# Kernel tuning notes

Hardware: AMD Instinct MI355X
Metric: run time of the kernel (lower is better)

## Reference

```python
import jax, jax.numpy as jnp
import numpy as np

WIN = 7       # window_size (square)
SHIFT = 3     # shift_size
HEADS = 4
WS = WIN * WIN  # 49 tokens per window


def _rel_index():
    # Swin relative position index, shape (WS*WS,), static ints
    coords = np.stack(np.meshgrid(np.arange(WIN), np.arange(WIN), indexing='ij'))
    cf = coords.reshape(2, -1)
    rel = (cf[:, :, None] - cf[:, None, :]).transpose(1, 2, 0)  # (WS, WS, 2)
    rel[:, :, 0] += WIN - 1
    rel[:, :, 1] += WIN - 1
    rel[:, :, 0] *= 2 * WIN - 1
    return rel.sum(-1).reshape(-1)

_REL_IDX = jnp.asarray(_rel_index())


def _attn_mask(H, W):
    # shift mask per window, shape (num_windows, WS, WS), static
    m = np.zeros((H, W), np.float32)
    cnt = 0
    for h in ((0, -WIN), (-WIN, -SHIFT), (-SHIFT, None)):
        for w in ((0, -WIN), (-WIN, -SHIFT), (-SHIFT, None)):
            m[h[0]:h[1], w[0]:w[1]] = cnt
            cnt += 1
    m = m.reshape(H // WIN, WIN, W // WIN, WIN).transpose(0, 2, 1, 3).reshape(-1, WS)
    diff = m[:, None, :] - m[:, :, None]
    return np.where(diff == 0, 0.0, -100.0).astype(np.float32)


def setup_inputs() -> dict:
    key = jax.random.key(0)
    ks = jax.random.split(key, 6)
    C = 128
    return {
        'x': jax.random.normal(ks[0], (64, 56, 56, C), jnp.float32),
        'qkv_kernel': jax.random.normal(ks[1], (C, 3 * C), jnp.float32) * (C ** -0.5),
        'qkv_bias': jax.random.normal(ks[2], (3 * C,), jnp.float32) * 0.02,
        'proj_kernel': jax.random.normal(ks[3], (C, C), jnp.float32) * (C ** -0.5),
        'proj_bias': jax.random.normal(ks[4], (C,), jnp.float32) * 0.02,
        'rel_pos_table': jax.random.normal(ks[5], ((2 * WIN - 1) ** 2, HEADS), jnp.float32) * 0.02,
    }


def reference(x, qkv_kernel, qkv_bias, proj_kernel, proj_bias, rel_pos_table):
    B, H, W, C = x.shape
    nH, nW = H // WIN, W // WIN
    head_dim = C // HEADS

    # cyclic shift + window partition -> (B*nH*nW, WS, C)
    xs = jnp.roll(x, (-SHIFT, -SHIFT), axis=(1, 2))
    xw = xs.reshape(B, nH, WIN, nW, WIN, C).transpose(0, 1, 3, 2, 4, 5).reshape(B * nH * nW, WS, C)

    qkv = xw @ qkv_kernel + qkv_bias
    qkv = qkv.reshape(-1, WS, 3, HEADS, head_dim).transpose(2, 0, 3, 1, 4)  # (3, n, h, WS, d)
    q, k, v = qkv[0], qkv[1], qkv[2]

    attn = jnp.einsum('nhsd,nhtd->nhst', q * head_dim ** -0.5, k)

    # relative position bias: (1, heads, WS, WS)
    bias = rel_pos_table[_REL_IDX].reshape(WS, WS, HEADS).transpose(2, 0, 1)[None]
    attn = attn + bias

    # shift mask (static)
    mask = jnp.asarray(_attn_mask(H, W))  # (nH*nW, WS, WS)
    attn = attn.reshape(B, nH * nW, HEADS, WS, WS) + mask[None, :, None]
    attn = jax.nn.softmax(attn.reshape(-1, HEADS, WS, WS), axis=-1)

    out = jnp.einsum('nhst,nhtd->nhsd', attn, v).transpose(0, 2, 1, 3).reshape(-1, WS, C)
    out = out @ proj_kernel + proj_bias

    # window merge + reverse shift
    out = out.reshape(B, nH, nW, WIN, WIN, C).transpose(0, 1, 3, 2, 4, 5).reshape(B, H, W, C)
    return jnp.roll(out, (SHIFT, SHIFT), axis=(1, 2))
```

## Files before the change

### kernel.cpp

```cpp
#include <hip/hip_runtime.h>
#include <hip/hip_bf16.h>

#define WIN 7
#define SHIFT_SZ 3
#define WSQ 49
#define CH 128
#define HW 56
#define LOG2E 1.4426950408889634f
#define QSCALE (0.17677669529663687f * LOG2E)

typedef short s16x8 __attribute__((ext_vector_type(8)));
typedef short s16x4 __attribute__((ext_vector_type(4)));
typedef float f32x4 __attribute__((ext_vector_type(4)));


__global__ void prep_weights(const float* __restrict__ qkv_kernel,
                             const float* __restrict__ proj_kernel,
                             __hip_bfloat16* __restrict__ ws) {
  int idx = blockIdx.x * 256 + threadIdx.x;
  if (idx < 49152) {
    int n = idx >> 7, c = idx & 127;
    ws[idx] = __float2bfloat16(qkv_kernel[c * 384 + n]);
  }
  if (idx < 16384) {
    int n = idx >> 7, c = idx & 127;
    ws[49152 + idx] = __float2bfloat16(proj_kernel[c * 128 + n]);
  }
}

__global__ void prep_tbl(const float* __restrict__ rel_pos_table,
                         __hip_bfloat16* __restrict__ tbl) {
  int idx = blockIdx.x * 256 + threadIdx.x;
  int t = idx & 63;
  int s = (idx >> 6) & 63;
  int h = (idx >> 12) & 3;
  int cls = idx >> 14;
  float v;
  if (t >= WSQ) v = -43280.f;
  else if (s >= WSQ) v = 0.f;
  else {
    int i1 = s / 7, j1 = s % 7, i2 = t / 7, j2 = t % 7;
    int ridx = (i1 - i2 + 6) * 13 + (j1 - j2 + 6);
    float bias = rel_pos_table[ridx * 4 + h];
    int wyIs7 = cls >> 1, wxIs7 = cls & 1;
    int rh1 = wyIs7 ? (i1 < 4 ? 1 : 2) : 0;
    int rh2 = wyIs7 ? (i2 < 4 ? 1 : 2) : 0;
    int rw1 = wxIs7 ? (j1 < 4 ? 1 : 2) : 0;
    int rw2 = wxIs7 ? (j2 < 4 ? 1 : 2) : 0;
    float mask = (rh1 == rh2 && rw1 == rw2) ? 0.f : -100.f;
    v = (bias + mask) * LOG2E;
  }
  tbl[idx] = __float2bfloat16(v);
}


static __device__ __forceinline__ s16x8 ld2x64(const __hip_bfloat16* p) {
  s16x8 r;
  *(s16x4*)&r = *(const s16x4*)p;
  *(((s16x4*)&r) + 1) = *(const s16x4*)(p + 4);
  return r;
}

__launch_bounds__(512, 6)
__global__ void swin_attn(const float* __restrict__ x,
                          const float* __restrict__ qkv_bias,
                          const float* __restrict__ proj_bias,
                          const __hip_bfloat16* __restrict__ wqkvT,
                          const __hip_bfloat16* __restrict__ wprojT,
                          const __hip_bfloat16* __restrict__ tbl,
                          float* __restrict__ out) {
  __shared__ __align__(16) char smem[53248];
  __hip_bfloat16* a_lds  = (__hip_bfloat16*)smem;
  __hip_bfloat16* q_lds  = (__hip_bfloat16*)smem;
  __hip_bfloat16* k_lds  = (__hip_bfloat16*)(smem + 18432);
  __hip_bfloat16* vt_lds = (__hip_bfloat16*)(smem + 36864);
  __hip_bfloat16* p_lds  = (__hip_bfloat16*)smem;
  __hip_bfloat16* o_lds  = (__hip_bfloat16*)(smem + 36864);

  const int tid = threadIdx.x;
  const int lane = tid & 63;
  const int wv = tid >> 6;
  const int g = lane >> 4;
  const int c = lane & 15;
  const int e = c & 7;

  const int widx = blockIdx.x;
  const int b  = widx >> 6;
  const int wy = (widx >> 3) & 7;
  const int wx = widx & 7;
  const int mc = ((wy == 7) ? 2 : 0) + ((wx == 7) ? 1 : 0);

  for (int it = tid; it < 1024; it += 512) {
    int s = it >> 4;
    int l16 = it & 15;
    union { s16x8 v; __hip_bfloat16 h[8]; } u;
    if (s < WSQ) {
      int i = s / 7, j = s - i * 7;
      int hh = wy * 7 + i + SHIFT_SZ; if (hh >= HW) hh -= HW;
      int ww = wx * 7 + j + SHIFT_SZ; if (ww >= HW) ww -= HW;
      const float4* src = (const float4*)(x + (((b * HW + hh) * HW + ww) * CH + l16 * 8));
      float4 f0 = src[0], f1 = src[1];
      u.h[0] = __float2bfloat16(f0.x); u.h[1] = __float2bfloat16(f0.y);
      u.h[2] = __float2bfloat16(f0.z); u.h[3] = __float2bfloat16(f0.w);
      u.h[4] = __float2bfloat16(f1.x); u.h[5] = __float2bfloat16(f1.y);
      u.h[6] = __float2bfloat16(f1.z); u.h[7] = __float2bfloat16(f1.w);
    } else {
      #pragma unroll
      for (int q = 0; q < 8; ++q) u.h[q] = __float2bfloat16(0.f);
    }
    *(s16x8*)(a_lds + s * 128 + ((l16 ^ (s & 7)) * 8)) = u.v;
  }
  __syncthreads();

  {
    f32x4 acc_v[4];
    #pragma unroll
    for (int mt = 0; mt < 4; ++mt) acc_v[mt] = (f32x4){0.f, 0.f, 0.f, 0.f};
    #pragma unroll
    for (int kt = 0; kt < 4; ++kt) {
      s16x8 bv = *(const s16x8*)(wqkvT + (16 * (16 + wv) + c) * 128 + kt * 32 + g * 8);
      #pragma unroll
      for (int mt = 0; mt < 4; ++mt) {
        s16x8 af = *(const s16x8*)(a_lds + (16 * mt + c) * 128 + ((4 * kt + g) ^ e) * 8);
        acc_v[mt] = __builtin_amdgcn_mfma_f32_16x16x32_bf16(af, bv, acc_v[mt], 0, 0, 0);
      }
    }
    int hv = wv >> 1;
    int d = (wv & 1) * 16 + c;
    float bvb = qkv_bias[256 + wv * 16 + c];
    __hip_bfloat16* vdst = vt_lds + (hv * 32 + d) * 64;
    #pragma unroll
    for (int mt = 0; mt < 4; ++mt) {
      union { s16x4 v; __hip_bfloat16 h[4]; } u;
      #pragma unroll
      for (int r = 0; r < 4; ++r) u.h[r] = __float2bfloat16(acc_v[mt][r] + bvb);
      *(s16x4*)(vdst + ((2 * mt + (g >> 1)) ^ e) * 8 + (g & 1) * 4) = u.v;
    }
  }

  {
    f32x4 acc[2][4];
    #pragma unroll
    for (int ntl = 0; ntl < 2; ++ntl)
      #pragma unroll
      for (int mt = 0; mt < 4; ++mt) acc[ntl][mt] = (f32x4){0.f, 0.f, 0.f, 0.f};
    #pragma unroll
    for (int kt = 0; kt < 4; ++kt) {
      s16x8 af[4];
      #pragma unroll
      for (int mt = 0; mt < 4; ++mt)
        af[mt] = *(const s16x8*)(a_lds + (16 * mt + c) * 128 + ((4 * kt + g) ^ e) * 8);
      #pragma unroll
      for (int ntl = 0; ntl < 2; ++ntl) {
        s16x8 bf = *(const s16x8*)(wqkvT + (16 * (2 * wv + ntl) + c) * 128 + kt * 32 + g * 8);
        #pragma unroll
        for (int mt = 0; mt < 4; ++mt)
          acc[ntl][mt] = __builtin_amdgcn_mfma_f32_16x16x32_bf16(bf, af[mt], acc[ntl][mt], 0, 0, 0);
      }
    }
    const float scale = (wv < 4) ? QSCALE : 1.0f;
    if (wv >= 4) {
      #pragma unroll
      for (int ntl = 0; ntl < 2; ++ntl) {
        int qt = 2 * wv + ntl;
        int h = (qt >> 1) & 3;
        int d0 = (qt & 1) * 16 + 4 * g;
        float4 b4 = *(const float4*)(qkv_bias + qt * 16 + 4 * g);
        __hip_bfloat16* dst = k_lds + h * 2304 + d0;
        #pragma unroll
        for (int mt = 0; mt < 4; ++mt) {
          union { s16x4 v; __hip_bfloat16 h[4]; } u;
          u.h[0] = __float2bfloat16((acc[ntl][mt][0] + b4.x) * scale);
          u.h[1] = __float2bfloat16((acc[ntl][mt][1] + b4.y) * scale);
          u.h[2] = __float2bfloat16((acc[ntl][mt][2] + b4.z) * scale);
          u.h[3] = __float2bfloat16((acc[ntl][mt][3] + b4.w) * scale);
          *(s16x4*)(dst + (16 * mt + c) * 36) = u.v;
        }
      }
    }
    __syncthreads();
    if (wv < 4) {
      #pragma unroll
      for (int ntl = 0; ntl < 2; ++ntl) {
        int qt = 2 * wv + ntl;
        int h = (qt >> 1) & 3;
        int d0 = (qt & 1) * 16 + 4 * g;
        float4 b4 = *(const float4*)(qkv_bias + qt * 16 + 4 * g);
        __hip_bfloat16* dst = q_lds + h * 2304 + d0;
        #pragma unroll
        for (int mt = 0; mt < 4; ++mt) {
          union { s16x4 v; __hip_bfloat16 h[4]; } u;
          u.h[0] = __float2bfloat16((acc[ntl][mt][0] + b4.x) * scale);
          u.h[1] = __float2bfloat16((acc[ntl][mt][1] + b4.y) * scale);
          u.h[2] = __float2bfloat16((acc[ntl][mt][2] + b4.z) * scale);
          u.h[3] = __float2bfloat16((acc[ntl][mt][3] + b4.w) * scale);
          *(s16x4*)(dst + (16 * mt + c) * 36) = u.v;
        }
      }
    }
  }
  __syncthreads();

  const int h3 = wv >> 1;
  const int mh = wv & 1;
  s16x8 qf[2], kf[4];
  #pragma unroll
  for (int m = 0; m < 2; ++m)
    qf[m] = ld2x64(q_lds + (h3 * 64 + 16 * (2 * mh + m) + c) * 36 + g * 8);
  #pragma unroll
  for (int nt = 0; nt < 4; ++nt)
    kf[nt] = ld2x64(k_lds + (h3 * 64 + 16 * nt + c) * 36 + g * 8);
  __syncthreads();

  #pragma unroll
  for (int m = 0; m < 2; ++m) {
    f32x4 sc[4];
    #pragma unroll
    for (int nt = 0; nt < 4; ++nt) {
      sc[nt] = (f32x4){0.f, 0.f, 0.f, 0.f};
      sc[nt] = __builtin_amdgcn_mfma_f32_16x16x32_bf16(kf[nt], qf[m], sc[nt], 0, 0, 0);
    }
    const __hip_bfloat16* tb_ =
        tbl + (((mc << 2) + h3) << 12) + (32 * mh + 16 * m + c) * 64;
    #pragma unroll
    for (int nt = 0; nt < 4; ++nt) {
      union { s16x4 v; __hip_bfloat16 h[4]; } tv;
      tv.v = *(const s16x4*)(tb_ + 16 * nt + 4 * g);
      #pragma unroll
      for (int r = 0; r < 4; ++r) sc[nt][r] += __bfloat162float(tv.h[r]);
    }
    float mx = -1e30f;
    #pragma unroll
    for (int nt = 0; nt < 4; ++nt)
      #pragma unroll
      for (int r = 0; r < 4; ++r) mx = fmaxf(mx, sc[nt][r]);
    mx = fmaxf(mx, __shfl_xor(mx, 16));
    mx = fmaxf(mx, __shfl_xor(mx, 32));
    float sum = 0.f;
    #pragma unroll
    for (int nt = 0; nt < 4; ++nt)
      #pragma unroll
      for (int r = 0; r < 4; ++r) {
        float e2 = __builtin_amdgcn_exp2f(sc[nt][r] - mx);
        sc[nt][r] = e2;
        sum += e2;
      }
    sum += __shfl_xor(sum, 16);
    sum += __shfl_xor(sum, 32);
    float inv = __builtin_amdgcn_rcpf(sum);
    __hip_bfloat16* prow = p_lds + (h3 * 64 + 16 * (2 * mh + m) + c) * 64;
    #pragma unroll
    for (int nt = 0; nt < 4; ++nt) {
      union { s16x4 v; __hip_bfloat16 h[4]; } u;
      #pragma unroll
      for (int r = 0; r < 4; ++r) u.h[r] = __float2bfloat16(sc[nt][r] * inv);
      *(s16x4*)(prow + ((2 * nt + (g >> 1)) ^ e) * 8 + (g & 1) * 4) = u.v;
    }
  }

  f32x4 oacc[2][2];
  #pragma unroll
  for (int m = 0; m < 2; ++m)
    #pragma unroll
    for (int ntd = 0; ntd < 2; ++ntd) oacc[m][ntd] = (f32x4){0.f, 0.f, 0.f, 0.f};
  #pragma unroll
  for (int kt = 0; kt < 2; ++kt) {
    s16x8 vfr[2], pfr[2];
    #pragma unroll
    for (int ntd = 0; ntd < 2; ++ntd)
      vfr[ntd] = *(const s16x8*)(vt_lds + (h3 * 32 + 16 * ntd + c) * 64 +
                                 (((4 * kt + g) ^ e) * 8));
    #pragma unroll
    for (int m = 0; m < 2; ++m)
      pfr[m] = *(const s16x8*)(p_lds + (h3 * 64 + 16 * (2 * mh + m) + c) * 64 +
                               (((4 * kt + g) ^ e) * 8));
    #pragma unroll
    for (int m = 0; m < 2; ++m)
      #pragma unroll
      for (int ntd = 0; ntd < 2; ++ntd)
        oacc[m][ntd] = __builtin_amdgcn_mfma_f32_16x16x32_bf16(vfr[ntd], pfr[m], oacc[m][ntd], 0, 0, 0);
  }
  __syncthreads();

  #pragma unroll
  for (int m = 0; m < 2; ++m)
    #pragma unroll
    for (int ntd = 0; ntd < 2; ++ntd) {
      union { s16x4 v; __hip_bfloat16 h[4]; } u;
      #pragma unroll
      for (int r = 0; r < 4; ++r) u.h[r] = __float2bfloat16(oacc[m][ntd][r]);
      *(s16x4*)(o_lds + (32 * mh + 16 * m + c) * 128 +
                ((4 * h3 + 2 * ntd + (g >> 1)) ^ e) * 8 + (g & 1) * 4) = u.v;
    }
  __syncthreads();

  {
    f32x4 pacc[4];
    #pragma unroll
    for (int mt = 0; mt < 4; ++mt) pacc[mt] = (f32x4){0.f, 0.f, 0.f, 0.f};
    #pragma unroll
    for (int kt = 0; kt < 4; ++kt) {
      s16x8 bfp = *(const s16x8*)(wprojT + (16 * wv + c) * 128 + kt * 32 + g * 8);
      #pragma unroll
      for (int mt = 0; mt < 4; ++mt) {
        s16x8 afo = *(const s16x8*)(o_lds + (16 * mt + c) * 128 + ((4 * kt + g) ^ e) * 8);
        pacc[mt] = __builtin_amdgcn_mfma_f32_16x16x32_bf16(bfp, afo, pacc[mt], 0, 0, 0);
      }
    }
    float4 pb4 = *(const float4*)(proj_bias + 16 * wv + 4 * g);
    #pragma unroll
    for (int mt = 0; mt < 4; ++mt) {
      int s = 16 * mt + c;
      if (s < WSQ) {
        int i = s / 7, j = s - i * 7;
        int hh = wy * 7 + i + SHIFT_SZ; if (hh >= HW) hh -= HW;
        int ww = wx * 7 + j + SHIFT_SZ; if (ww >= HW) ww -= HW;
        float4 v;
        v.x = pacc[mt][0] + pb4.x;
        v.y = pacc[mt][1] + pb4.y;
        v.z = pacc[mt][2] + pb4.z;
        v.w = pacc[mt][3] + pb4.w;
        *(float4*)(out + ((b * HW + hh) * HW + ww) * CH + 16 * wv + 4 * g) = v;
      }
    }
  }
}

extern "C" void kernel_launch(void* const* d_in, const int* in_sizes, int n_in,
                              void* d_out, int out_size, void* d_ws, size_t ws_size,
                              hipStream_t stream) {
  const float* x            = (const float*)d_in[0];
  const float* qkv_kernel   = (const float*)d_in[1];
  const float* qkv_bias     = (const float*)d_in[2];
  const float* proj_kernel  = (const float*)d_in[3];
  const float* proj_bias    = (const float*)d_in[4];
  const float* rel_pos_tbl  = (const float*)d_in[5];
  float* out = (float*)d_out;

  __hip_bfloat16* wsb    = (__hip_bfloat16*)d_ws;
  __hip_bfloat16* wqkvT  = wsb;
  __hip_bfloat16* wprojT = wsb + 49152;
  __hip_bfloat16* tbl    = wsb + 65536;

  prep_weights<<<dim3(192), dim3(256), 0, stream>>>(qkv_kernel, proj_kernel, wsb);
  prep_tbl<<<dim3(256), dim3(256), 0, stream>>>(rel_pos_tbl, tbl);
  swin_attn<<<dim3(4096), dim3(512), 0, stream>>>(x, qkv_bias, proj_bias,
                                                  wqkvT, wprojT, tbl, out);
}
```

Baseline: 126.8 us.

## Split fused window attention into QKV kernel and attention kernel via global scratch

Splits the single fused kernel into two. The first computes the QKV projection and writes Q, K and V as bf16 MFMA-fragment-layout tiles to workspace. The second uses 256-thread blocks that load those fragments straight into registers, run attention with 16x16x16 MFMAs and softmax, then do the output projection. The goal is to cut LDS use per block and the syncs between stages so occupancy rises, at the cost of an extra round trip through global memory of about 100MB. The fused path is kept as a fallback when the workspace is too small.

```diff
diff --git a/kernel.cpp b/kernel.cpp
--- a/kernel.cpp
+++ b/kernel.cpp
@@ -12,6 +12,16 @@
 typedef short s16x8 __attribute__((ext_vector_type(8)));
 typedef short s16x4 __attribute__((ext_vector_type(4)));
 typedef float f32x4 __attribute__((ext_vector_type(4)));
+
+static __device__ __forceinline__ f32x4 mfma16(s16x4 a, s16x4 b, f32x4 c) {
+#if __has_builtin(__builtin_amdgcn_mfma_f32_16x16x16bf16_1k)
+  return __builtin_amdgcn_mfma_f32_16x16x16bf16_1k(a, b, c, 0, 0, 0);
+#else
+  f32x4 d;
+  asm("v_mfma_f32_16x16x16_bf16 %0, %1, %2, %3" : "=v"(d) : "v"(a), "v"(b), "v"(c));
+  return d;
+#endif
+}
 
 
 __global__ void prep_weights(const float* __restrict__ qkv_kernel,
@@ -54,28 +64,15 @@
 }
 
 
-static __device__ __forceinline__ s16x8 ld2x64(const __hip_bfloat16* p) {
-  s16x8 r;
-  *(s16x4*)&r = *(const s16x4*)p;
-  *(((s16x4*)&r) + 1) = *(const s16x4*)(p + 4);
-  return r;
-}
-
 __launch_bounds__(512, 6)
-__global__ void swin_attn(const float* __restrict__ x,
-                          const float* __restrict__ qkv_bias,
-                          const float* __restrict__ proj_bias,
-                          const __hip_bfloat16* __restrict__ wqkvT,
-                          const __hip_bfloat16* __restrict__ wprojT,
-                          const __hip_bfloat16* __restrict__ tbl,
-                          float* __restrict__ out) {
-  __shared__ __align__(16) char smem[53248];
-  __hip_bfloat16* a_lds  = (__hip_bfloat16*)smem;
-  __hip_bfloat16* q_lds  = (__hip_bfloat16*)smem;
-  __hip_bfloat16* k_lds  = (__hip_bfloat16*)(smem + 18432);
-  __hip_bfloat16* vt_lds = (__hip_bfloat16*)(smem + 36864);
-  __hip_bfloat16* p_lds  = (__hip_bfloat16*)smem;
-  __hip_bfloat16* o_lds  = (__hip_bfloat16*)(smem + 36864);
+__global__ void qkv_win(const float* __restrict__ x,
+                        const float* __restrict__ qkv_bias,
+                        const __hip_bfloat16* __restrict__ wqkvT,
+                        __hip_bfloat16* __restrict__ qg,
+                        __hip_bfloat16* __restrict__ kg,
+                        __hip_bfloat16* __restrict__ vg) {
+  __shared__ __align__(16) char smem[16384];
+  __hip_bfloat16* a_lds = (__hip_bfloat16*)smem;
 
   const int tid = threadIdx.x;
   const int lane = tid & 63;
@@ -88,7 +85,6 @@
   const int b  = widx >> 6;
   const int wy = (widx >> 3) & 7;
   const int wx = widx & 7;
-  const int mc = ((wy == 7) ? 2 : 0) + ((wx == 7) ? 1 : 0);
 
   for (int it = tid; it < 1024; it += 512) {
     int s = it >> 4;
@@ -126,6 +122,266 @@
       }
     }
     int hv = wv >> 1;
+    int vt = wv & 1;
+    float bvb = qkv_bias[256 + wv * 16 + c];
+    __hip_bfloat16* vdst = vg + (((widx * 4 + hv) * 2 + vt) * 16 + c) * 64;
+    #pragma unroll
+    for (int mt = 0; mt < 4; ++mt) {
+      union { s16x4 v; __hip_bfloat16 h[4]; } u;
+      #pragma unroll
+      for (int r = 0; r < 4; ++r) u.h[r] = __float2bfloat16(acc_v[mt][r] + bvb);
+      *(s16x4*)(vdst + mt * 16 + g * 4) = u.v;
+    }
+  }
+
+  {
+    f32x4 acc[2][4];
+    #pragma unroll
+    for (int ntl = 0; ntl < 2; ++ntl)
+      #pragma unroll
+      for (int mt = 0; mt < 4; ++mt) acc[ntl][mt] = (f32x4){0.f, 0.f, 0.f, 0.f};
+    #pragma unroll
+    for (int kt = 0; kt < 4; ++kt) {
+      s16x8 af[4];
+      #pragma unroll
+      for (int mt = 0; mt < 4; ++mt)
+        af[mt] = *(const s16x8*)(a_lds + (16 * mt + c) * 128 + ((4 * kt + g) ^ e) * 8);
+      #pragma unroll
+      for (int ntl = 0; ntl < 2; ++ntl) {
+        s16x8 bf = *(const s16x8*)(wqkvT + (16 * (2 * wv + ntl) + c) * 128 + kt * 32 + g * 8);
+        #pragma unroll
+        for (int mt = 0; mt < 4; ++mt)
+          acc[ntl][mt] = __builtin_amdgcn_mfma_f32_16x16x32_bf16(bf, af[mt], acc[ntl][mt], 0, 0, 0);
+      }
+    }
+    const float scale = (wv < 4) ? QSCALE : 1.0f;
+    #pragma unroll
+    for (int ntl = 0; ntl < 2; ++ntl) {
+      int qt = 2 * wv + ntl;
+      int head = (qt >> 1) & 3;
+      int kb = qt & 1;
+      float4 b4 = *(const float4*)(qkv_bias + qt * 16 + 4 * g);
+      __hip_bfloat16* dst = (qt < 8 ? qg : kg) + ((widx * 4 + head) * 2 + kb) * 1024;
+      #pragma unroll
+      for (int mt = 0; mt < 4; ++mt) {
+        union { s16x4 v; __hip_bfloat16 h[4]; } u;
+        u.h[0] = __float2bfloat16((acc[ntl][mt][0] + b4.x) * scale);
+        u.h[1] = __float2bfloat16((acc[ntl][mt][1] + b4.y) * scale);
+        u.h[2] = __float2bfloat16((acc[ntl][mt][2] + b4.z) * scale);
+        u.h[3] = __float2bfloat16((acc[ntl][mt][3] + b4.w) * scale);
+        *(s16x4*)(dst + (16 * mt + c) * 16 + g * 4) = u.v;
+      }
+    }
+  }
+}
+
+
+__launch_bounds__(256, 5)
+__global__ void attn_win(const float* __restrict__ proj_bias,
+                         const __hip_bfloat16* __restrict__ wprojT,
+                         const __hip_bfloat16* __restrict__ tbl,
+                         const __hip_bfloat16* __restrict__ qg,
+                         const __hip_bfloat16* __restrict__ kg,
+                         const __hip_bfloat16* __restrict__ vg,
+                         float* __restrict__ out) {
+  __shared__ __align__(16) char smem[16384];
+  __hip_bfloat16* o_lds = (__hip_bfloat16*)smem;
+
+  const int tid = threadIdx.x;
+  const int lane = tid & 63;
+  const int wv = tid >> 6;
+  const int g = lane >> 4;
+  const int c = lane & 15;
+  const int e = c & 7;
+
+  const int widx = blockIdx.x;
+  const int b  = widx >> 6;
+  const int wy = (widx >> 3) & 7;
+  const int wx = widx & 7;
+  const int mc = ((wy == 7) ? 2 : 0) + ((wx == 7) ? 1 : 0);
+
+  s16x4 kf16[2][4];
+  const __hip_bfloat16* kbase = kg + (widx * 4 + wv) * 2048;
+  #pragma unroll
+  for (int kb = 0; kb < 2; ++kb)
+    #pragma unroll
+    for (int nt = 0; nt < 4; ++nt)
+      kf16[kb][nt] = *(const s16x4*)(kbase + kb * 1024 + (16 * nt + c) * 16 + g * 4);
+  s16x4 vf16[2][4];
+  const __hip_bfloat16* vbase = vg + (widx * 4 + wv) * 2048;
+  #pragma unroll
+  for (int vt = 0; vt < 2; ++vt)
+    #pragma unroll
+    for (int mt = 0; mt < 4; ++mt)
+      vf16[vt][mt] = *(const s16x4*)(vbase + vt * 1024 + c * 64 + mt * 16 + g * 4);
+
+  const __hip_bfloat16* qbase = qg + (widx * 4 + wv) * 2048;
+
+  #pragma unroll 1
+  for (int m = 0; m < 4; ++m) {
+    s16x4 qf[2];
+    #pragma unroll
+    for (int kb = 0; kb < 2; ++kb)
+      qf[kb] = *(const s16x4*)(qbase + kb * 1024 + (16 * m + c) * 16 + g * 4);
+    const __hip_bfloat16* tb_ =
+        tbl + (((mc << 2) + wv) << 12) + (16 * m + c) * 64;
+    union { s16x4 v; __hip_bfloat16 h[4]; } tv[4];
+    #pragma unroll
+    for (int nt = 0; nt < 4; ++nt) tv[nt].v = *(const s16x4*)(tb_ + 16 * nt + 4 * g);
+    f32x4 sc[4];
+    #pragma unroll
+    for (int nt = 0; nt < 4; ++nt) {
+      sc[nt] = (f32x4){0.f, 0.f, 0.f, 0.f};
+      #pragma unroll
+      for (int kb = 0; kb < 2; ++kb)
+        sc[nt] = mfma16(kf16[kb][nt], qf[kb], sc[nt]);
+    }
+    #pragma unroll
+    for (int nt = 0; nt < 4; ++nt)
+      #pragma unroll
+      for (int r = 0; r < 4; ++r) sc[nt][r] += __bfloat162float(tv[nt].h[r]);
+    float mx = -1e30f;
+    #pragma unroll
+    for (int nt = 0; nt < 4; ++nt)
+      #pragma unroll
+      for (int r = 0; r < 4; ++r) mx = fmaxf(mx, sc[nt][r]);
+    mx = fmaxf(mx, __shfl_xor(mx, 16));
+    mx = fmaxf(mx, __shfl_xor(mx, 32));
+    float sum = 0.f;
+    #pragma unroll
+    for (int nt = 0; nt < 4; ++nt)
+      #pragma unroll
+      for (int r = 0; r < 4; ++r) {
+        float ex = __builtin_amdgcn_exp2f(sc[nt][r] - mx);
+        sc[nt][r] = ex;
+        sum += ex;
+      }
+    s16x4 pf[4];
+    #pragma unroll
+    for (int nt = 0; nt < 4; ++nt) {
+      union { s16x4 v; __hip_bfloat16 h[4]; } u;
+      #pragma unroll
+      for (int r = 0; r < 4; ++r) u.h[r] = __float2bfloat16(sc[nt][r]);
+      pf[nt] = u.v;
+    }
+    sum += __shfl_xor(sum, 16);
+    sum += __shfl_xor(sum, 32);
+    float inv = __builtin_amdgcn_rcpf(sum);
+    #pragma unroll
+    for (int vt = 0; vt < 2; ++vt) {
+      f32x4 oacc = (f32x4){0.f, 0.f, 0.f, 0.f};
+      #pragma unroll
+      for (int nt = 0; nt < 4; ++nt)
+        oacc = mfma16(vf16[vt][nt], pf[nt], oacc);
+      union { s16x4 v; __hip_bfloat16 h[4]; } u;
+      #pragma unroll
+      for (int r = 0; r < 4; ++r) u.h[r] = __float2bfloat16(oacc[r] * inv);
+      *(s16x4*)(o_lds + (16 * m + c) * 128 +
+                ((4 * wv + 2 * vt + (g >> 1)) ^ e) * 8 + (g & 1) * 4) = u.v;
+    }
+  }
+  __syncthreads();
+
+  #pragma unroll
+  for (int ntl = 0; ntl < 2; ++ntl) {
+    int nt = 2 * wv + ntl;
+    float4 pb4 = *(const float4*)(proj_bias + 16 * nt + 4 * g);
+    f32x4 pacc[4];
+    #pragma unroll
+    for (int mt = 0; mt < 4; ++mt) pacc[mt] = (f32x4){pb4.x, pb4.y, pb4.z, pb4.w};
+    #pragma unroll
+    for (int kt = 0; kt < 4; ++kt) {
+      s16x8 bfp = *(const s16x8*)(wprojT + (16 * nt + c) * 128 + kt * 32 + g * 8);
+      #pragma unroll
+      for (int mt = 0; mt < 4; ++mt) {
+        s16x8 afo = *(const s16x8*)(o_lds + (16 * mt + c) * 128 + ((4 * kt + g) ^ e) * 8);
+        pacc[mt] = __builtin_amdgcn_mfma_f32_16x16x32_bf16(bfp, afo, pacc[mt], 0, 0, 0);
+      }
+    }
+    #pragma unroll
+    for (int mt = 0; mt < 4; ++mt) {
+      int s = 16 * mt + c;
+      if (s < WSQ) {
+        int i = s / 7, j = s - i * 7;
+        int hh = wy * 7 + i + SHIFT_SZ; if (hh >= HW) hh -= HW;
+        int ww = wx * 7 + j + SHIFT_SZ; if (ww >= HW) ww -= HW;
+        float4 v;
+        v.x = pacc[mt][0];
+        v.y = pacc[mt][1];
+        v.z = pacc[mt][2];
+        v.w = pacc[mt][3];
+        *(float4*)(out + ((b * HW + hh) * HW + ww) * CH + 16 * nt + 4 * g) = v;
+      }
+    }
+  }
+}
+
+
+__launch_bounds__(512, 6)
+__global__ void swin_attn_fused(const float* __restrict__ x,
+                                const float* __restrict__ qkv_bias,
+                                const float* __restrict__ proj_bias,
+                                const __hip_bfloat16* __restrict__ wqkvT,
+                                const __hip_bfloat16* __restrict__ wprojT,
+                                const __hip_bfloat16* __restrict__ tbl,
+                                float* __restrict__ out) {
+  __shared__ __align__(16) char smem[53248];
+  __hip_bfloat16* a_lds  = (__hip_bfloat16*)smem;
+  __hip_bfloat16* q_lds  = (__hip_bfloat16*)smem;
+  __hip_bfloat16* k_lds  = (__hip_bfloat16*)(smem + 18432);
+  __hip_bfloat16* vt_lds = (__hip_bfloat16*)(smem + 36864);
+  __hip_bfloat16* p_lds  = (__hip_bfloat16*)smem;
+  __hip_bfloat16* o_lds  = (__hip_bfloat16*)(smem + 36864);
+
+  const int tid = threadIdx.x;
+  const int lane = tid & 63;
+  const int wv = tid >> 6;
+  const int g = lane >> 4;
+  const int c = lane & 15;
+  const int e = c & 7;
+
+  const int widx = blockIdx.x;
+  const int b  = widx >> 6;
+  const int wy = (widx >> 3) & 7;
+  const int wx = widx & 7;
+  const int mc = ((wy == 7) ? 2 : 0) + ((wx == 7) ? 1 : 0);
+
+  for (int it = tid; it < 1024; it += 512) {
+    int s = it >> 4;
+    int l16 = it & 15;
+    union { s16x8 v; __hip_bfloat16 h[8]; } u;
+    if (s < WSQ) {
+      int i = s / 7, j = s - i * 7;
+      int hh = wy * 7 + i + SHIFT_SZ; if (hh >= HW) hh -= HW;
+      int ww = wx * 7 + j + SHIFT_SZ; if (ww >= HW) ww -= HW;
+      const float4* src = (const float4*)(x + (((b * HW + hh) * HW + ww) * CH + l16 * 8));
+      float4 f0 = src[0], f1 = src[1];
+      u.h[0] = __float2bfloat16(f0.x); u.h[1] = __float2bfloat16(f0.y);
+      u.h[2] = __float2bfloat16(f0.z); u.h[3] = __float2bfloat16(f0.w);
+      u.h[4] = __float2bfloat16(f1.x); u.h[5] = __float2bfloat16(f1.y);
+      u.h[6] = __float2bfloat16(f1.z); u.h[7] = __float2bfloat16(f1.w);
+    } else {
+      #pragma unroll
+      for (int q = 0; q < 8; ++q) u.h[q] = __float2bfloat16(0.f);
+    }
+    *(s16x8*)(a_lds + s * 128 + ((l16 ^ (s & 7)) * 8)) = u.v;
+  }
+  __syncthreads();
+
+  {
+    f32x4 acc_v[4];
+    #pragma unroll
+    for (int mt = 0; mt < 4; ++mt) acc_v[mt] = (f32x4){0.f, 0.f, 0.f, 0.f};
+    #pragma unroll
+    for (int kt = 0; kt < 4; ++kt) {
+      s16x8 bv = *(const s16x8*)(wqkvT + (16 * (16 + wv) + c) * 128 + kt * 32 + g * 8);
+      #pragma unroll
+      for (int mt = 0; mt < 4; ++mt) {
+        s16x8 af = *(const s16x8*)(a_lds + (16 * mt + c) * 128 + ((4 * kt + g) ^ e) * 8);
+        acc_v[mt] = __builtin_amdgcn_mfma_f32_16x16x32_bf16(af, bv, acc_v[mt], 0, 0, 0);
+      }
+    }
+    int hv = wv >> 1;
     int d = (wv & 1) * 16 + c;
     float bvb = qkv_bias[256 + wv * 16 + c];
     __hip_bfloat16* vdst = vt_lds + (hv * 32 + d) * 64;
@@ -205,11 +461,17 @@
   const int mh = wv & 1;
   s16x8 qf[2], kf[4];
   #pragma unroll
-  for (int m = 0; m < 2; ++m)
-    qf[m] = ld2x64(q_lds + (h3 * 64 + 16 * (2 * mh + m) + c) * 36 + g * 8);
-  #pragma unroll
-  for (int nt = 0; nt < 4; ++nt)
-    kf[nt] = ld2x64(k_lds + (h3 * 64 + 16 * nt + c) * 36 + g * 8);
+  for (int m = 0; m < 2; ++m) {
+    const __hip_bfloat16* p = q_lds + (h3 * 64 + 16 * (2 * mh + m) + c) * 36 + g * 8;
+    *(s16x4*)&qf[m] = *(const s16x4*)p;
+    *(((s16x4*)&qf[m]) + 1) = *(const s16x4*)(p + 4);
+  }
+  #pragma unroll
+  for (int nt = 0; nt < 4; ++nt) {
+    const __hip_bfloat16* p = k_lds + (h3 * 64 + 16 * nt + c) * 36 + g * 8;
+    *(s16x4*)&kf[nt] = *(const s16x4*)p;
+    *(((s16x4*)&kf[nt]) + 1) = *(const s16x4*)(p + 4);
+  }
   __syncthreads();
 
   #pragma unroll
@@ -344,6 +606,18 @@
 
   prep_weights<<<dim3(192), dim3(256), 0, stream>>>(qkv_kernel, proj_kernel, wsb);
   prep_tbl<<<dim3(256), dim3(256), 0, stream>>>(rel_pos_tbl, tbl);
-  swin_attn<<<dim3(4096), dim3(512), 0, stream>>>(x, qkv_bias, proj_bias,
-                                                  wqkvT, wprojT, tbl, out);
+
+  const size_t frag_elems = (size_t)4096 * 4 * 2 * 1024;
+  const size_t need_bytes = (131072 + 3 * frag_elems) * 2;
+  if (ws_size >= need_bytes) {
+    __hip_bfloat16* qg = wsb + 131072;
+    __hip_bfloat16* kg = qg + frag_elems;
+    __hip_bfloat16* vg = kg + frag_elems;
+    qkv_win<<<dim3(4096), dim3(512), 0, stream>>>(x, qkv_bias, wqkvT, qg, kg, vg);
+    attn_win<<<dim3(4096), dim3(256), 0, stream>>>(proj_bias, wprojT, tbl,
+                                                   qg, kg, vg, out);
+  } else {
+    swin_attn_fused<<<dim3(4096), dim3(512), 0, stream>>>(x, qkv_bias, proj_bias,
+                                                          wqkvT, wprojT, tbl, out);
+  }
 }
```

New measurement: 194.0 us. +53.0%, slower.

## Keep softmax probabilities in registers and feed PV MFMA directly

Applied to the files above, without the earlier changes.

Probabilities are no longer written to LDS and read back. The unnormalized exponentials are converted to bf16 register fragments and consumed by 16x16x16 bf16 MFMAs against V fragments preloaded into registers. Normalization by the row sum moves to after the PV product, and one barrier plus the P staging round trip are removed. In exchange it uses more, smaller MFMA instructions and more registers for the V fragments, and O now aliases the Q region.

```diff
diff --git a/kernel.cpp b/kernel.cpp
--- a/kernel.cpp
+++ b/kernel.cpp
@@ -12,6 +12,16 @@
 typedef short s16x8 __attribute__((ext_vector_type(8)));
 typedef short s16x4 __attribute__((ext_vector_type(4)));
 typedef float f32x4 __attribute__((ext_vector_type(4)));
+
+static __device__ __forceinline__ f32x4 mfma16(s16x4 a, s16x4 b, f32x4 c) {
+#if __has_builtin(__builtin_amdgcn_mfma_f32_16x16x16bf16_1k)
+  return __builtin_amdgcn_mfma_f32_16x16x16bf16_1k(a, b, c, 0, 0, 0);
+#else
+  f32x4 d;
+  asm("v_mfma_f32_16x16x16_bf16 %0, %1, %2, %3" : "=v"(d) : "v"(a), "v"(b), "v"(c));
+  return d;
+#endif
+}
 
 
 __global__ void prep_weights(const float* __restrict__ qkv_kernel,
@@ -54,13 +64,6 @@
 }
 
 
-static __device__ __forceinline__ s16x8 ld2x64(const __hip_bfloat16* p) {
-  s16x8 r;
-  *(s16x4*)&r = *(const s16x4*)p;
-  *(((s16x4*)&r) + 1) = *(const s16x4*)(p + 4);
-  return r;
-}
-
 __launch_bounds__(512, 6)
 __global__ void swin_attn(const float* __restrict__ x,
                           const float* __restrict__ qkv_bias,
@@ -74,8 +77,7 @@
   __hip_bfloat16* q_lds  = (__hip_bfloat16*)smem;
   __hip_bfloat16* k_lds  = (__hip_bfloat16*)(smem + 18432);
   __hip_bfloat16* vt_lds = (__hip_bfloat16*)(smem + 36864);
-  __hip_bfloat16* p_lds  = (__hip_bfloat16*)smem;
-  __hip_bfloat16* o_lds  = (__hip_bfloat16*)(smem + 36864);
+  __hip_bfloat16* o_lds  = (__hip_bfloat16*)smem;
 
   const int tid = threadIdx.x;
   const int lane = tid & 63;
@@ -205,12 +207,26 @@
   const int mh = wv & 1;
   s16x8 qf[2], kf[4];
   #pragma unroll
-  for (int m = 0; m < 2; ++m)
-    qf[m] = ld2x64(q_lds + (h3 * 64 + 16 * (2 * mh + m) + c) * 36 + g * 8);
+  for (int m = 0; m < 2; ++m) {
+    const __hip_bfloat16* p = q_lds + (h3 * 64 + 16 * (2 * mh + m) + c) * 36 + g * 8;
+    *(s16x4*)&qf[m] = *(const s16x4*)p;
+    *(((s16x4*)&qf[m]) + 1) = *(const s16x4*)(p + 4);
+  }
   #pragma unroll
-  for (int nt = 0; nt < 4; ++nt)
-    kf[nt] = ld2x64(k_lds + (h3 * 64 + 16 * nt + c) * 36 + g * 8);
+  for (int nt = 0; nt < 4; ++nt) {
+    const __hip_bfloat16* p = k_lds + (h3 * 64 + 16 * nt + c) * 36 + g * 8;
+    *(s16x4*)&kf[nt] = *(const s16x4*)p;
+    *(((s16x4*)&kf[nt]) + 1) = *(const s16x4*)(p + 4);
+  }
   __syncthreads();
+
+  s16x4 vf16[2][4];
+  #pragma unroll
+  for (int vt = 0; vt < 2; ++vt)
+    #pragma unroll
+    for (int nt = 0; nt < 4; ++nt)
+      vf16[vt][nt] = *(const s16x4*)(vt_lds + (h3 * 32 + 16 * vt + c) * 64 +
+                                     ((2 * nt + (g >> 1)) ^ e) * 8 + (g & 1) * 4);
 
   #pragma unroll
   for (int m = 0; m < 2; ++m) {
@@ -241,57 +257,34 @@
     for (int nt = 0; nt < 4; ++nt)
       #pragma unroll
       for (int r = 0; r < 4; ++r) {
-        float e2 = __builtin_amdgcn_exp2f(sc[nt][r] - mx);
-        sc[nt][r] = e2;
-        sum += e2;
-      }
+        float ex = __builtin_amdgcn_exp2f(sc[nt][r] - mx);
+        sc[nt][r] = ex;
+        sum += ex;
+      }
+    s16x4 pf[4];
+    #pragma unroll
+    for (int nt = 0; nt < 4; ++nt) {
+      union { s16x4 v; __hip_bfloat16 h[4]; } u;
+      #pragma unroll
+      for (int r = 0; r < 4; ++r) u.h[r] = __float2bfloat16(sc[nt][r]);
+      pf[nt] = u.v;
+    }
     sum += __shfl_xor(sum, 16);
     sum += __shfl_xor(sum, 32);
     float inv = __builtin_amdgcn_rcpf(sum);
-    __hip_bfloat16* prow = p_lds + (h3 * 64 + 16 * (2 * mh + m) + c) * 64;
-    #pragma unroll
-    for (int nt = 0; nt < 4; ++nt) {
+    #pragma unroll
+    for (int vt = 0; vt < 2; ++vt) {
+      f32x4 oacc = (f32x4){0.f, 0.f, 0.f, 0.f};
+      #pragma unroll
+      for (int nt = 0; nt < 4; ++nt)
+        oacc = mfma16(vf16[vt][nt], pf[nt], oacc);
       union { s16x4 v; __hip_bfloat16 h[4]; } u;
       #pragma unroll
-      for (int r = 0; r < 4; ++r) u.h[r] = __float2bfloat16(sc[nt][r] * inv);
-      *(s16x4*)(prow + ((2 * nt + (g >> 1)) ^ e) * 8 + (g & 1) * 4) = u.v;
-    }
-  }
-
-  f32x4 oacc[2][2];
-  #pragma unroll
-  for (int m = 0; m < 2; ++m)
-    #pragma unroll
-    for (int ntd = 0; ntd < 2; ++ntd) oacc[m][ntd] = (f32x4){0.f, 0.f, 0.f, 0.f};
-  #pragma unroll
-  for (int kt = 0; kt < 2; ++kt) {
-    s16x8 vfr[2], pfr[2];
-    #pragma unroll
-    for (int ntd = 0; ntd < 2; ++ntd)
-      vfr[ntd] = *(const s16x8*)(vt_lds + (h3 * 32 + 16 * ntd + c) * 64 +
-                                 (((4 * kt + g) ^ e) * 8));
-    #pragma unroll
-    for (int m = 0; m < 2; ++m)
-      pfr[m] = *(const s16x8*)(p_lds + (h3 * 64 + 16 * (2 * mh + m) + c) * 64 +
-                               (((4 * kt + g) ^ e) * 8));
-    #pragma unroll
-    for (int m = 0; m < 2; ++m)
-      #pragma unroll
-      for (int ntd = 0; ntd < 2; ++ntd)
-        oacc[m][ntd] = __builtin_amdgcn_mfma_f32_16x16x32_bf16(vfr[ntd], pfr[m], oacc[m][ntd], 0, 0, 0);
-  }
-  __syncthreads();
-
-  #pragma unroll
-  for (int m = 0; m < 2; ++m)
-    #pragma unroll
-    for (int ntd = 0; ntd < 2; ++ntd) {
-      union { s16x4 v; __hip_bfloat16 h[4]; } u;
-      #pragma unroll
-      for (int r = 0; r < 4; ++r) u.h[r] = __float2bfloat16(oacc[m][ntd][r]);
+      for (int r = 0; r < 4; ++r) u.h[r] = __float2bfloat16(oacc[r] * inv);
       *(s16x4*)(o_lds + (32 * mh + 16 * m + c) * 128 +
-                ((4 * h3 + 2 * ntd + (g >> 1)) ^ e) * 8 + (g & 1) * 4) = u.v;
-    }
+                ((4 * h3 + 2 * vt + (g >> 1)) ^ e) * 8 + (g & 1) * 4) = u.v;
+    }
+  }
   __syncthreads();
 
   {
```

New measurement: 136.7 us. +7.7%, slower.
